# Performance work log

Measured on AMD Instinct MI355X. Metric: run time of the kernel, lower is better.

## Reference

```python
import jax, jax.numpy as jnp
import numpy as np

B, TASK, LQ, D = 16, 80, 1024, 768
HH, HD, P, NL = 12, 64, 4, 1
HF, WF = 64, 64
LIN = HF * WF
EPS = 1e-6


def _ln(x, w, b):
    mu = jnp.mean(x, -1, keepdims=True)
    var = jnp.mean(jnp.square(x - mu), -1, keepdims=True)
    return (x - mu) * jax.lax.rsqrt(var + EPS) * w + b


def _bilinear(value_l, loc_l, Hl, Wl):
    # value_l: [B, HH, S, HD]; loc_l: [B, LQ, HH, P, 2] in [0,1]
    # replicates F.grid_sample(align_corners=False, padding_mode='zeros')
    b, hh, s, hd = value_l.shape
    lq, p = loc_l.shape[1], loc_l.shape[3]
    x = loc_l[..., 0] * Wl - 0.5
    y = loc_l[..., 1] * Hl - 0.5
    x0 = jnp.floor(x)
    y0 = jnp.floor(y)
    out = jnp.zeros((b, hh, lq, p, hd), value_l.dtype)
    for dx in (0, 1):
        for dy in (0, 1):
            xc = x0 + dx
            yc = y0 + dy
            w = (1.0 - jnp.abs(x - xc)) * (1.0 - jnp.abs(y - yc))
            valid = (xc >= 0) & (xc <= Wl - 1) & (yc >= 0) & (yc <= Hl - 1)
            w = jnp.where(valid, w, 0.0)
            xi = jnp.clip(xc, 0, Wl - 1).astype(jnp.int32)
            yi = jnp.clip(yc, 0, Hl - 1).astype(jnp.int32)
            lin = (yi * Wl + xi).transpose(0, 2, 1, 3).reshape(b, hh, lq * p, 1)
            v = jnp.take_along_axis(value_l, lin, axis=2).reshape(b, hh, lq, p, hd)
            out = out + v * w.transpose(0, 2, 1, 3)[..., None]
    return out


def _forward(query, reference_points, feat, spatial_shapes, level_start_index,
             qn_w, qn_b, fn_w, fn_b, gamma,
             W_off, b_off, W_attw, b_attw, W_val, b_val, W_out, b_out):
    ss = np.asarray(spatial_shapes)
    lsi = np.asarray(level_start_index)
    tt = query[:, :TASK]
    q = query[:, TASK:]
    bq, lq, _ = q.shape
    qn = _ln(q, qn_w, qn_b)
    fn = _ln(feat, fn_w, fn_b)
    # value projection: [B, Lin, D] -> [B, HH, Lin, HD]
    value = (fn @ W_val + b_val).reshape(bq, -1, HH, HD).transpose(0, 2, 1, 3)
    off = (qn @ W_off + b_off).reshape(bq, lq, HH, NL, P, 2)
    aw = (qn @ W_attw + b_attw).reshape(bq, lq, HH, NL * P)
    aw = jax.nn.softmax(aw, axis=-1).reshape(bq, lq, HH, NL, P)
    # offset normalizer is [W, H] per level
    norm = jnp.stack([ss[:, 1].astype(jnp.float32), ss[:, 0].astype(jnp.float32)], -1)
    loc = reference_points[:, :, None, :, None, :] + off / norm[None, None, None, :, None, :]
    out = jnp.zeros((bq, lq, HH, HD), query.dtype)
    for l in range(ss.shape[0]):
        Hl, Wl = int(ss[l, 0]), int(ss[l, 1])
        st = int(lsi[l])
        vl = value[:, :, st:st + Hl * Wl]
        sampled = _bilinear(vl, loc[:, :, :, l], Hl, Wl)  # [B,HH,LQ,P,HD]
        out = out + jnp.einsum('bhqpd,bqhp->bqhd', sampled, aw[:, :, :, l])
    attn = out.reshape(bq, lq, HH * HD) @ W_out + b_out
    q = q + gamma * attn
    return jnp.concatenate([tt, q], axis=1)


def setup_inputs():
    key = jax.random.key(0)
    ks = jax.random.split(key, 10)
    s = 0.02
    return {
        "query": jax.random.normal(ks[0], (B, TASK + LQ, D), jnp.float32),
        "reference_points": jax.random.uniform(ks[1], (B, LQ, NL, 2), dtype=jnp.float32),
        "feat": jax.random.normal(ks[2], (B, LIN, D), jnp.float32),
        "spatial_shapes": jnp.array([[HF, WF]], jnp.int32),
        "level_start_index": jnp.array([0], jnp.int32),
        "qn_w": jnp.ones((D,), jnp.float32),
        "qn_b": jnp.zeros((D,), jnp.float32),
        "fn_w": jnp.ones((D,), jnp.float32),
        "fn_b": jnp.zeros((D,), jnp.float32),
        "gamma": 0.1 * jax.random.normal(ks[3], (D,), jnp.float32),
        "W_off": s * jax.random.normal(ks[4], (D, HH * NL * P * 2), jnp.float32),
        "b_off": s * jax.random.normal(ks[5], (HH * NL * P * 2,), jnp.float32),
        "W_attw": s * jax.random.normal(ks[6], (D, HH * NL * P), jnp.float32),
        "b_attw": s * jax.random.normal(ks[7], (HH * NL * P,), jnp.float32),
        "W_val": s * jax.random.normal(ks[8], (D, D), jnp.float32),
        "b_val": jnp.zeros((D,), jnp.float32),
        "W_out": s * jax.random.normal(ks[9], (D, D), jnp.float32),
        "b_out": jnp.zeros((D,), jnp.float32),
    }


def reference(query, reference_points, feat, spatial_shapes, level_start_index, qn_w, qn_b, fn_w, fn_b, gamma, W_off, b_off, W_attw, b_attw, W_val, b_val, W_out, b_out):
    return _forward(query, reference_points, feat, spatial_shapes, level_start_index,
                    qn_w, qn_b, fn_w, fn_b, gamma,
                    W_off, b_off, W_attw, b_attw, W_val, b_val, W_out, b_out)
```

## Files before the change

### kernel.cpp

```cpp
#include <hip/hip_runtime.h>
#include <hip/hip_bf16.h>

using bf16 = __hip_bfloat16;
typedef __attribute__((ext_vector_type(8))) short short8;
typedef __attribute__((ext_vector_type(4))) short short4v;
typedef __attribute__((ext_vector_type(4))) float floatx4;

#define B_    16
#define TASK_ 80
#define LQ_   1024
#define D_    768
#define HH_   12
#define HD_   64
#define LIN_  4096
#define MQ_   (B_*LQ_)
#define MF_   (B_*LIN_)
#define QR_   (TASK_+LQ_)

static constexpr size_t OFF_VAL = 0;
static constexpr size_t OFF_FN  = OFF_VAL + (size_t)MF_*D_*2;
static constexpr size_t OFF_QN  = OFF_FN  + (size_t)MF_*D_*2;
static constexpr size_t OFF_OA  = OFF_QN  + (size_t)MQ_*D_*2;
static constexpr size_t OFF_WVT = OFF_OA  + (size_t)MQ_*144*4;
static constexpr size_t OFF_WOT = OFF_WVT + (size_t)D_*D_*2;
static constexpr size_t OFF_WCT = OFF_WOT + (size_t)D_*D_*2;

__device__ __forceinline__ void async16(const void* g, void* l) {
  __builtin_amdgcn_global_load_lds((const __attribute__((address_space(1))) void*)g,
                                   (__attribute__((address_space(3))) void*)l, 16, 0, 0);
}

__global__ __launch_bounds__(256) void k_weights(const float* __restrict__ Wv, const float* __restrict__ Wo,
                                                 const float* __restrict__ Woff, const float* __restrict__ Wat,
                                                 bf16* __restrict__ WvT, bf16* __restrict__ WoT,
                                                 bf16* __restrict__ WcT) {
  int bid = blockIdx.x;
  if (bid < 288) {
    const float* W = (bid < 144) ? Wv : Wo;
    bf16* WT = (bid < 144) ? WvT : WoT;
    int lb = (bid < 144) ? bid : bid - 144;
    __shared__ float t[64][65];
    int bx = lb % 12, by = lb / 12;
    int n0 = bx*64, k0 = by*64;
    int col = threadIdx.x & 63, rg = threadIdx.x >> 6;
    #pragma unroll
    for (int i=0;i<16;++i) { int row = i*4+rg; t[row][col] = W[(size_t)(k0+row)*D_ + n0+col]; }
    __syncthreads();
    #pragma unroll
    for (int i=0;i<16;++i) { int row = i*4+rg; WT[(size_t)(n0+row)*D_ + k0+col] = __float2bfloat16(t[col][row]); }
  } else {
    int idx = (bid-288)*256 + threadIdx.x;
    int j = idx / D_, k = idx - j*D_;
    float v = 0.f;
    if (j < 96)       v = Woff[(size_t)k*96 + j];
    else if (j < 144) v = Wat[(size_t)k*48 + (j-96)];
    WcT[idx] = __float2bfloat16(v);
  }
}

__global__ __launch_bounds__(256) void k_ln(const float* __restrict__ query, const float* __restrict__ feat,
                                            const float* __restrict__ qw, const float* __restrict__ qb,
                                            const float* __restrict__ fw, const float* __restrict__ fb,
                                            bf16* __restrict__ qn, bf16* __restrict__ fn) {
  int r = blockIdx.x*4 + (threadIdx.x>>6);
  int lane = threadIdx.x & 63;
  const float* src; const float* w; const float* bia; bf16* dst;
  if (r < MQ_) {
    int bat = r >> 10, rr = r & 1023;
    src = query + ((size_t)bat*QR_ + TASK_ + rr)*D_;
    w = qw; bia = qb; dst = qn + (size_t)r*D_;
  } else {
    int fr = r - MQ_;
    src = feat + (size_t)fr*D_;
    w = fw; bia = fb; dst = fn + (size_t)fr*D_;
  }
  float4 v[3];
  #pragma unroll
  for (int j=0;j<3;++j) v[j] = ((const float4*)src)[lane + 64*j];
  float s = 0.f, s2 = 0.f;
  #pragma unroll
  for (int j=0;j<3;++j) {
    s  += v[j].x + v[j].y + v[j].z + v[j].w;
    s2 += v[j].x*v[j].x + v[j].y*v[j].y + v[j].z*v[j].z + v[j].w*v[j].w;
  }
  #pragma unroll
  for (int o=32;o>0;o>>=1){ s += __shfl_xor(s,o); s2 += __shfl_xor(s2,o); }
  float mu  = s*(1.f/D_);
  float var = s2*(1.f/D_) - mu*mu;
  float rstd = rsqrtf(var + 1e-6f);
  #pragma unroll
  for (int j=0;j<3;++j) {
    float4 ww = ((const float4*)w)[lane + 64*j];
    float4 bb = ((const float4*)bia)[lane + 64*j];
    short4v o4;
    o4[0] = (short)__bfloat16_as_ushort(__float2bfloat16((v[j].x-mu)*rstd*ww.x + bb.x));
    o4[1] = (short)__bfloat16_as_ushort(__float2bfloat16((v[j].y-mu)*rstd*ww.y + bb.y));
    o4[2] = (short)__bfloat16_as_ushort(__float2bfloat16((v[j].z-mu)*rstd*ww.z + bb.z));
    o4[3] = (short)__bfloat16_as_ushort(__float2bfloat16((v[j].w-mu)*rstd*ww.w + bb.w));
    *(short4v*)(dst + 4*(lane + 64*j)) = o4;
  }
}

__global__ __launch_bounds__(512, 2) void k_gemm_val(const bf16* __restrict__ A, const bf16* __restrict__ BT,
                                                     const float* __restrict__ bias0, bf16* __restrict__ outp) {
  __shared__ char lds[98304];
  const int K = D_;
  const int tid = threadIdx.x, wid = tid>>6, lane = tid&63;
  const int nwg = gridDim.x*gridDim.y;
  const int d = blockIdx.y*gridDim.x + blockIdx.x;
  const int logical = (d & 7)*(nwg>>3) + (d>>3);
  const int bm = (logical/3)*256, bn = (logical%3)*256;
  const int wm = wid>>2, wn = wid&3;
  const int srow = tid>>2;
  const int sslot = ((tid&3) ^ ((tid>>3)&3))*8;
  const bf16* gA0 = A  + (size_t)(bm + srow)*K + sslot;
  const bf16* gA1 = A  + (size_t)(bm + 128 + srow)*K + sslot;
  const bf16* gB0 = BT + (size_t)(bn + srow)*K + sslot;
  const bf16* gB1 = BT + (size_t)(bn + 128 + srow)*K + sslot;
  const int dstbase = (tid>>6)<<10;
  const int rb = (lane&15)*64 + ((((lane>>4) ^ ((lane>>1)&3)))<<4);
  floatx4 acc[8][4] = {};
  auto stageAll = [&](int k0, char* buf) {
    async16(gA0+k0, buf + dstbase);
    async16(gA1+k0, buf + 8192 + dstbase);
    async16(gB0+k0, buf + 16384 + dstbase);
    async16(gB1+k0, buf + 24576 + dstbase);
  };
  stageAll(0,  lds);
  stageAll(32, lds + 32768);
  const int NT = K >> 5;
  int cur = 0, nxt = 2;
  for (int k = 0; k < NT; ++k) {
    if (k < NT-1) asm volatile("s_waitcnt vmcnt(4)" ::: "memory");
    else          asm volatile("s_waitcnt vmcnt(0)" ::: "memory");
    __builtin_amdgcn_s_barrier();
    __builtin_amdgcn_sched_barrier(0);
    const int kk = (k+2)*32;
    const bool pf = (k+2 < NT);
    const char* lA = lds + cur*32768;
    const char* lB = lA + 16384;
    char* bufn = lds + nxt*32768;
    short8 af[8], bfr[4];
    if (pf) async16(gA0+kk, bufn + dstbase);
    #pragma unroll
    for (int i=0;i<4;++i) af[i] = *(const short8*)(lA + (wm*128 + i*16)*64 + rb);
    #pragma unroll
    for (int i=0;i<2;++i) bfr[i] = *(const short8*)(lB + (wn*64 + i*16)*64 + rb);
    __builtin_amdgcn_s_barrier();
    __builtin_amdgcn_s_setprio(1);
    #pragma unroll
    for (int mi=0;mi<4;++mi)
      #pragma unroll
      for (int ni=0;ni<2;++ni)
        acc[mi][ni] = __builtin_amdgcn_mfma_f32_16x16x32_bf16(af[mi], bfr[ni], acc[mi][ni], 0, 0, 0);
    __builtin_amdgcn_s_setprio(0);
    __builtin_amdgcn_s_barrier();
    __builtin_amdgcn_sched_barrier(0);
    if (pf) async16(gA1+kk, bufn + 8192 + dstbase);
    #pragma unroll
    for (int i=2;i<4;++i) bfr[i] = *(const short8*)(lB + (wn*64 + i*16)*64 + rb);
    __builtin_amdgcn_s_barrier();
    __builtin_amdgcn_s_setprio(1);
    #pragma unroll
    for (int mi=0;mi<4;++mi)
      #pragma unroll
      for (int ni=2;ni<4;++ni)
        acc[mi][ni] = __builtin_amdgcn_mfma_f32_16x16x32_bf16(af[mi], bfr[ni], acc[mi][ni], 0, 0, 0);
    __builtin_amdgcn_s_setprio(0);
    __builtin_amdgcn_s_barrier();
    __builtin_amdgcn_sched_barrier(0);
    if (pf) async16(gB0+kk, bufn + 16384 + dstbase);
    #pragma unroll
    for (int i=4;i<8;++i) af[i] = *(const short8*)(lA + (wm*128 + i*16)*64 + rb);
    __builtin_amdgcn_s_barrier();
    __builtin_amdgcn_s_setprio(1);
    #pragma unroll
    for (int mi=4;mi<8;++mi)
      #pragma unroll
      for (int ni=0;ni<2;++ni)
        acc[mi][ni] = __builtin_amdgcn_mfma_f32_16x16x32_bf16(af[mi], bfr[ni], acc[mi][ni], 0, 0, 0);
    __builtin_amdgcn_s_setprio(0);
    __builtin_amdgcn_s_barrier();
    __builtin_amdgcn_sched_barrier(0);
    if (pf) async16(gB1+kk, bufn + 24576 + dstbase);
    __builtin_amdgcn_s_barrier();
    __builtin_amdgcn_s_setprio(1);
    #pragma unroll
    for (int mi=4;mi<8;++mi)
      #pragma unroll
      for (int ni=2;ni<4;++ni)
        acc[mi][ni] = __builtin_amdgcn_mfma_f32_16x16x32_bf16(af[mi], bfr[ni], acc[mi][ni], 0, 0, 0);
    __builtin_amdgcn_s_setprio(0);
    __builtin_amdgcn_sched_barrier(0);
    cur = (cur==2) ? 0 : cur+1;
    nxt = (nxt==2) ? 0 : nxt+1;
  }
  const int rowb = (lane>>4)*4, col = lane&15;
  #pragma unroll
  for (int mi=0;mi<8;++mi) {
    #pragma unroll
    for (int ni=0;ni<4;++ni) {
      const int gn = bn + wn*64 + ni*16 + col;
      const float bv = bias0[gn];
      const int h = gn >> 6, hd = gn & 63;
      #pragma unroll
      for (int r=0;r<4;++r) {
        const int gm = bm + wm*128 + mi*16 + rowb + r;
        const int b = gm >> 12, pix = gm & 4095;
        outp[(((size_t)(b*HH_+h)*LIN_ + pix)<<6) + hd] = __float2bfloat16(acc[mi][ni][r] + bv);
      }
    }
  }
}

template<int MODE>
__global__ __launch_bounds__(256) void k_gemm(const bf16* __restrict__ A, const bf16* __restrict__ BT,
                                              int K,
                                              const float* __restrict__ bias0, const float* __restrict__ bias1,
                                              void* __restrict__ outp,
                                              const float* __restrict__ query, const float* __restrict__ gamma) {
  __shared__ char lds[49152];
  const int tid = threadIdx.x, wid = tid>>6, lane = tid&63;
  const int nwg = gridDim.x*gridDim.y, ny = gridDim.y;
  const int d = blockIdx.y*gridDim.x + blockIdx.x;
  const int logical = (d & 7)*(nwg>>3) + (d>>3);
  const int bm = (logical/ny)*128, bn = (logical%ny)*128;
  const int wr = wid>>1, wc = wid&1;
  const int c0 = wid*2, c1 = c0+1;
  const int sr0 = c0*16 + (lane>>2), sr1 = sr0+16;
  const int skb = (((lane&3) ^ ((lane>>3)&3)))*8;
  const bf16* ga0 = A  + (size_t)(bm+sr0)*K + skb;
  const bf16* ga1 = A  + (size_t)(bm+sr1)*K + skb;
  const bf16* gb0 = BT + (size_t)(bn+sr0)*K + skb;
  const bf16* gb1 = BT + (size_t)(bn+sr1)*K + skb;
  const int rb = (lane&15)*64 + ((((lane>>4) ^ ((lane>>1)&3)))<<4);
  floatx4 acc[4][4] = {};
  auto stage = [&](int k0, char* buf) {
    char* dA = buf; char* dB = buf + 8192;
    async16(ga0+k0, dA + c0*1024); async16(ga1+k0, dA + c1*1024);
    async16(gb0+k0, dB + c0*1024); async16(gb1+k0, dB + c1*1024);
  };
  stage(0,  lds);
  stage(32, lds + 16384);
  const int NT = K >> 5;
  int cur = 0, nxt = 2;
  for (int k = 0; k < NT; ++k) {
    if (k < NT-1) asm volatile("s_waitcnt vmcnt(4)" ::: "memory");
    else          asm volatile("s_waitcnt vmcnt(0)" ::: "memory");
    __builtin_amdgcn_s_barrier();
    __builtin_amdgcn_sched_barrier(0);
    if (k + 2 < NT) stage((k+2)*32, lds + nxt*16384);
    const char* ldsA = lds + cur*16384; const char* ldsB = ldsA + 8192;
    short8 af[4], bfr[4];
    #pragma unroll
    for (int i=0;i<4;++i) {
      af[i]  = *(const short8*)(ldsA + (wr*64 + i*16)*64 + rb);
      bfr[i] = *(const short8*)(ldsB + (wc*64 + i*16)*64 + rb);
    }
    #pragma unroll
    for (int mi=0;mi<4;++mi)
      #pragma unroll
      for (int ni=0;ni<4;++ni)
        acc[mi][ni] = __builtin_amdgcn_mfma_f32_16x16x32_bf16(af[mi], bfr[ni], acc[mi][ni], 0, 0, 0);
    cur = (cur==2) ? 0 : cur+1;
    nxt = (nxt==2) ? 0 : nxt+1;
  }
  const int rowb = (lane>>4)*4, col = lane&15;
  #pragma unroll
  for (int mi=0;mi<4;++mi) {
    #pragma unroll
    for (int ni=0;ni<4;++ni) {
      const int gn = bn + wc*64 + ni*16 + col;
      #pragma unroll
      for (int r=0;r<4;++r) {
        const int gm = bm + wr*64 + mi*16 + rowb + r;
        float v = acc[mi][ni][r];
        if constexpr (MODE==1) {
          if (gn < 144) {
            v += (gn < 96) ? bias0[gn] : bias1[gn-96];
            ((float*)outp)[(size_t)gm*144 + gn] = v;
          }
        } else {
          v += bias0[gn];
          int b = gm >> 10, lq = gm & 1023;
          size_t idx = ((size_t)b*QR_ + TASK_ + lq)*D_ + gn;
          ((float*)outp)[idx] = query[idx] + gamma[gn]*v;
        }
      }
    }
  }
}

__global__ __launch_bounds__(256) void k_prep(const float* __restrict__ oa_all,
                                              const float* __restrict__ refp,
                                              float2* __restrict__ prep,
                                              const float* __restrict__ query, float* __restrict__ out) {
  int idx = blockIdx.x*256 + threadIdx.x;
  int p = idx & 3, mh = idx >> 2;
  int h = mh % HH_, m = mh / HH_;
  const float* oa = oa_all + (size_t)m*144;
  float l0 = oa[96+h*4+0], l1 = oa[96+h*4+1], l2 = oa[96+h*4+2], l3 = oa[96+h*4+3];
  float mx = fmaxf(fmaxf(l0,l1), fmaxf(l2,l3));
  float e0 = expf(l0-mx), e1 = expf(l1-mx), e2 = expf(l2-mx), e3 = expf(l3-mx);
  float inv = 1.f/(e0+e1+e2+e3);
  float ep = (p==0)?e0:(p==1)?e1:(p==2)?e2:e3;
  float awp = ep*inv;
  float x = refp[(size_t)m*2+0]*64.f - 0.5f + oa[h*8+p*2+0];
  float y = refp[(size_t)m*2+1]*64.f - 0.5f + oa[h*8+p*2+1];
  float x0f = floorf(x), y0f = floorf(y);
  int ix = (int)x0f, iy = (int)y0f;
  float fx = x-x0f, fy = y-y0f;
  float wx[2] = {1.f-fx, fx}, wy[2] = {1.f-fy, fy};
  float2 e[4];
  #pragma unroll
  for (int c=0;c<4;++c) {
    int dx = c&1, dy = c>>1;
    int xc = ix+dx, yc = iy+dy;
    bool valid = ((unsigned)xc < 64u) && ((unsigned)yc < 64u);
    float w = valid ? awp*wx[dx]*wy[dy] : 0.f;
    int xi = min(max(xc,0),63), yi = min(max(yc,0),63);
    e[c].x = w;
    e[c].y = __int_as_float(yi*64+xi);
  }
  float2* dst = prep + (size_t)mh*16 + p*4;
  *(float4*)(dst)   = make_float4(e[0].x, e[0].y, e[1].x, e[1].y);
  *(float4*)(dst+2) = make_float4(e[2].x, e[2].y, e[3].x, e[3].y);
  if (blockIdx.x < 960) {
    int ci = blockIdx.x*256 + threadIdx.x;
    const int perb = TASK_*D_/4;
    int b = ci / perb, r = ci - b*perb;
    const float4* s = (const float4*)(query + (size_t)b*QR_*D_) + r;
    float4* dd = (float4*)(out + (size_t)b*QR_*D_) + r;
    *dd = *s;
  }
}

__global__ __launch_bounds__(256) void k_sample(const float2* __restrict__ prep,
                                                const bf16* __restrict__ value,
                                                bf16* __restrict__ sampout) {
  int g  = blockIdx.x*8 + (threadIdx.x>>5);
  int l  = threadIdx.x & 31;
  int c8 = l >> 2, p = l & 3;
  int h = g % HH_, m = g / HH_;
  int b = m >> 10;
  const float2* pb = prep + (size_t)g*16 + p*4;
  float4 e01 = *(const float4*)(pb);
  float4 e23 = *(const float4*)(pb+2);
  const bf16* vb = value + (((size_t)(b*HH_+h))<<18) + (c8<<3);
  float a[8] = {};
  float wv[4]  = {e01.x, e01.z, e23.x, e23.z};
  int   pix[4] = {__float_as_int(e01.y), __float_as_int(e01.w),
                  __float_as_int(e23.y), __float_as_int(e23.w)};
  #pragma unroll
  for (int c=0;c<4;++c) {
    short8 v = *(const short8*)(vb + ((size_t)pix[c]<<6));
    float w = wv[c];
    #pragma unroll
    for (int j=0;j<8;++j)
      a[j] += w*__uint_as_float(((unsigned)(unsigned short)v[j])<<16);
  }
  #pragma unroll
  for (int j=0;j<8;++j) { a[j] += __shfl_xor(a[j],1); a[j] += __shfl_xor(a[j],2); }
  if (p == 0) {
    short8 o;
    #pragma unroll
    for (int j=0;j<8;++j)
      o[j] = (short)__bfloat16_as_ushort(__float2bfloat16(a[j]));
    *(short8*)(sampout + (size_t)m*D_ + h*64 + c8*8) = o;
  }
}

extern "C" void kernel_launch(void* const* d_in, const int* in_sizes, int n_in,
                              void* d_out, int out_size, void* d_ws, size_t ws_size,
                              hipStream_t stream) {
  (void)in_sizes; (void)n_in; (void)out_size; (void)ws_size;
  const float* query = (const float*)d_in[0];
  const float* refp  = (const float*)d_in[1];
  const float* feat  = (const float*)d_in[2];
  const float* qn_w  = (const float*)d_in[5];
  const float* qn_b  = (const float*)d_in[6];
  const float* fn_w  = (const float*)d_in[7];
  const float* fn_b  = (const float*)d_in[8];
  const float* gamma = (const float*)d_in[9];
  const float* W_off = (const float*)d_in[10];
  const float* b_off = (const float*)d_in[11];
  const float* W_attw= (const float*)d_in[12];
  const float* b_attw= (const float*)d_in[13];
  const float* W_val = (const float*)d_in[14];
  const float* b_val = (const float*)d_in[15];
  const float* W_out = (const float*)d_in[16];
  const float* b_out = (const float*)d_in[17];
  char*  ws  = (char*)d_ws;
  float* out = (float*)d_out;

  bf16*   wsVal  = (bf16*)(ws + OFF_VAL);
  bf16*   wsFn   = (bf16*)(ws + OFF_FN);
  bf16*   wsQn   = (bf16*)(ws + OFF_QN);
  float*  wsOA   = (float*)(ws + OFF_OA);
  bf16*   wsWvT  = (bf16*)(ws + OFF_WVT);
  bf16*   wsWoT  = (bf16*)(ws + OFF_WOT);
  bf16*   wsWcT  = (bf16*)(ws + OFF_WCT);
  float2* wsPrep = (float2*)(ws + OFF_QN);
  bf16*   wsSamp = wsFn;

  k_weights<<<1056, 256, 0, stream>>>(W_val, W_out, W_off, W_attw, wsWvT, wsWoT, wsWcT);
  k_ln<<<(MQ_+MF_)/4, 256, 0, stream>>>(query, feat, qn_w, qn_b, fn_w, fn_b, wsQn, wsFn);
  k_gemm<1><<<dim3(MQ_/128, 2), 256, 0, stream>>>(wsQn, wsWcT, D_, b_off, b_attw, wsOA, nullptr, nullptr);
  k_prep<<<(MQ_*HH_*4)/256, 256, 0, stream>>>(wsOA, refp, wsPrep, query, out);
  k_gemm_val<<<dim3(MF_/256, 3), 512, 0, stream>>>(wsFn, wsWvT, b_val, wsVal);
  k_sample<<<(MQ_*HH_)/8, 256, 0, stream>>>(wsPrep, wsVal, wsSamp);
  k_gemm<2><<<dim3(MQ_/128, 6), 256, 0, stream>>>(wsSamp, wsWoT, D_, b_out, nullptr, out, query, gamma);
}
```

Baseline: 275.9 us.

## Use 256x256 tiled GEMM for output projection and reorder sampling blocks by head

The output projection GEMM now runs on the larger 256x256-tile, 512-thread kernel already used for the value projection, templated to write the residual-gated fp32 output. The separate 128-tile kernel is reduced to the offset/attention-weight projection only. The sampling kernel remaps block indices so consecutive blocks handle the same head, with an XCD-style interleave, to improve cache locality on the value tensor. The output GEMM grid shrinks to 192 workgroups, which may underfill the GPU's compute units.

```diff
diff --git a/kernel.cpp b/kernel.cpp
--- a/kernel.cpp
+++ b/kernel.cpp
@@ -101,8 +101,10 @@
   }
 }
 
-__global__ __launch_bounds__(512, 2) void k_gemm_val(const bf16* __restrict__ A, const bf16* __restrict__ BT,
-                                                     const float* __restrict__ bias0, bf16* __restrict__ outp) {
+template<int MODE>
+__global__ __launch_bounds__(512, 2) void k_gemm256(const bf16* __restrict__ A, const bf16* __restrict__ BT,
+                                                    const float* __restrict__ bias0, void* __restrict__ outp,
+                                                    const float* __restrict__ query, const float* __restrict__ gamma) {
   __shared__ char lds[98304];
   const int K = D_;
   const int tid = threadIdx.x, wid = tid>>6, lane = tid&63;
@@ -202,23 +204,27 @@
     for (int ni=0;ni<4;++ni) {
       const int gn = bn + wn*64 + ni*16 + col;
       const float bv = bias0[gn];
-      const int h = gn >> 6, hd = gn & 63;
       #pragma unroll
       for (int r=0;r<4;++r) {
         const int gm = bm + wm*128 + mi*16 + rowb + r;
-        const int b = gm >> 12, pix = gm & 4095;
-        outp[(((size_t)(b*HH_+h)*LIN_ + pix)<<6) + hd] = __float2bfloat16(acc[mi][ni][r] + bv);
+        if constexpr (MODE==0) {
+          const int h = gn >> 6, hd = gn & 63;
+          const int b = gm >> 12, pix = gm & 4095;
+          ((bf16*)outp)[(((size_t)(b*HH_+h)*LIN_ + pix)<<6) + hd] = __float2bfloat16(acc[mi][ni][r] + bv);
+        } else {
+          const int bq = gm >> 10, lq = gm & 1023;
+          size_t idx = ((size_t)bq*QR_ + TASK_ + lq)*D_ + gn;
+          ((float*)outp)[idx] = query[idx] + gamma[gn]*(acc[mi][ni][r] + bv);
+        }
       }
     }
   }
 }
 
-template<int MODE>
-__global__ __launch_bounds__(256) void k_gemm(const bf16* __restrict__ A, const bf16* __restrict__ BT,
-                                              int K,
-                                              const float* __restrict__ bias0, const float* __restrict__ bias1,
-                                              void* __restrict__ outp,
-                                              const float* __restrict__ query, const float* __restrict__ gamma) {
+__global__ __launch_bounds__(256) void k_gemm1(const bf16* __restrict__ A, const bf16* __restrict__ BT,
+                                               int K,
+                                               const float* __restrict__ bias0, const float* __restrict__ bias1,
+                                               float* __restrict__ outp) {
   __shared__ char lds[49152];
   const int tid = threadIdx.x, wid = tid>>6, lane = tid&63;
   const int nwg = gridDim.x*gridDim.y, ny = gridDim.y;
@@ -275,16 +281,9 @@
       for (int r=0;r<4;++r) {
         const int gm = bm + wr*64 + mi*16 + rowb + r;
         float v = acc[mi][ni][r];
-        if constexpr (MODE==1) {
-          if (gn < 144) {
-            v += (gn < 96) ? bias0[gn] : bias1[gn-96];
-            ((float*)outp)[(size_t)gm*144 + gn] = v;
-          }
-        } else {
-          v += bias0[gn];
-          int b = gm >> 10, lq = gm & 1023;
-          size_t idx = ((size_t)b*QR_ + TASK_ + lq)*D_ + gn;
-          ((float*)outp)[idx] = query[idx] + gamma[gn]*v;
+        if (gn < 144) {
+          v += (gn < 96) ? bias0[gn] : bias1[gn-96];
+          outp[(size_t)gm*144 + gn] = v;
         }
       }
     }
@@ -338,12 +337,16 @@
 __global__ __launch_bounds__(256) void k_sample(const float2* __restrict__ prep,
                                                 const bf16* __restrict__ value,
                                                 bf16* __restrict__ sampout) {
-  int g  = blockIdx.x*8 + (threadIdx.x>>5);
+  const int nblk = (MQ_*HH_)/8;
+  int bid = blockIdx.x;
+  int logical = (bid & 7)*(nblk>>3) + (bid>>3);
+  int gi = logical*8 + (threadIdx.x>>5);
   int l  = threadIdx.x & 31;
   int c8 = l >> 2, p = l & 3;
-  int h = g % HH_, m = g / HH_;
+  int h = gi >> 14;
+  int m = gi & (MQ_-1);
   int b = m >> 10;
-  const float2* pb = prep + (size_t)g*16 + p*4;
+  const float2* pb = prep + ((size_t)m*HH_ + h)*16 + p*4;
   float4 e01 = *(const float4*)(pb);
   float4 e23 = *(const float4*)(pb+2);
   const bf16* vb = value + (((size_t)(b*HH_+h))<<18) + (c8<<3);
@@ -405,9 +408,9 @@
 
   k_weights<<<1056, 256, 0, stream>>>(W_val, W_out, W_off, W_attw, wsWvT, wsWoT, wsWcT);
   k_ln<<<(MQ_+MF_)/4, 256, 0, stream>>>(query, feat, qn_w, qn_b, fn_w, fn_b, wsQn, wsFn);
-  k_gemm<1><<<dim3(MQ_/128, 2), 256, 0, stream>>>(wsQn, wsWcT, D_, b_off, b_attw, wsOA, nullptr, nullptr);
+  k_gemm1<<<dim3(MQ_/128, 2), 256, 0, stream>>>(wsQn, wsWcT, D_, b_off, b_attw, wsOA);
   k_prep<<<(MQ_*HH_*4)/256, 256, 0, stream>>>(wsOA, refp, wsPrep, query, out);
-  k_gemm_val<<<dim3(MF_/256, 3), 512, 0, stream>>>(wsFn, wsWvT, b_val, wsVal);
+  k_gemm256<0><<<dim3(MF_/256, 3), 512, 0, stream>>>(wsFn, wsWvT, b_val, wsVal, nullptr, nullptr);
   k_sample<<<(MQ_*HH_)/8, 256, 0, stream>>>(wsPrep, wsVal, wsSamp);
-  k_gemm<2><<<dim3(MQ_/128, 6), 256, 0, stream>>>(wsSamp, wsWoT, D_, b_out, nullptr, out, query, gamma);
-}
+  k_gemm256<2><<<dim3(MQ_/256, 3), 512, 0, stream>>>(wsSamp, wsWoT, b_out, out, query, gamma);
+}
```

Measured after the change: 278.6 us. No clear change (+1.0%).
